# Optimization experiments

Hardware: AMD Instinct MI355X
Metric: run time of the kernel (lower is better)

## Reference

```python
import jax, jax.numpy as jnp
import numpy as np

D = 1024
H = 16
HD = D // H  # 64


def setup_inputs() -> dict:
    key = jax.random.key(0)
    ks = jax.random.split(key, 12)
    B, S = 2, 2048
    inp = {
        "input_query": jax.random.normal(ks[0], (B, S, D), jnp.float32),
        "input_key": jax.random.normal(ks[1], (B, S, D), jnp.float32),
        "input_value": jax.random.normal(ks[2], (B, S, D), jnp.float32),
        "mask": jnp.ones((S, S), dtype=bool),  # ignored, as in original
        # per-head Q/K/V linears, stacked over heads: [H, D, HD]
        "Wq": jax.random.normal(ks[3], (H, D, HD), jnp.float32) / np.sqrt(D),
        "bq": jax.random.normal(ks[4], (H, HD), jnp.float32) * 0.01,
        "Wk": jax.random.normal(ks[5], (H, D, HD), jnp.float32) / np.sqrt(D),
        "bk": jax.random.normal(ks[6], (H, HD), jnp.float32) * 0.01,
        "Wv": jax.random.normal(ks[7], (H, D, HD), jnp.float32) / np.sqrt(D),
        "bv": jax.random.normal(ks[8], (H, HD), jnp.float32) * 0.01,
        "Wo": jax.random.normal(ks[9], (D, D), jnp.float32) / np.sqrt(D),
        "bo": jax.random.normal(ks[10], (D,), jnp.float32) * 0.01,
    }
    return inp


def reference(input_query, input_key, input_value, mask, Wq, bq, Wk, bk, Wv, bv, Wo, bo):
    B, S, _ = input_query.shape
    # batched per-head projections: [B,S,D] x [H,D,HD] -> [B,H,S,HD]
    q = jnp.einsum("bsd,hdk->bhsk", input_query, Wq) + bq[None, :, None, :]
    k = jnp.einsum("bsd,hdk->bhsk", input_key, Wk) + bk[None, :, None, :]
    v = jnp.einsum("bsd,hdk->bhsk", input_value, Wv) + bv[None, :, None, :]
    scale = 1.0 / np.sqrt(HD)
    scores = jnp.einsum("bhqk,bhsk->bhqs", q, k) * scale  # [B,H,S,S]
    causal = jnp.tril(jnp.ones((S, S), dtype=bool))
    scores = jnp.where(causal[None, None], scores, jnp.finfo(scores.dtype).min)
    p = jax.nn.softmax(scores, axis=-1)
    out = jnp.einsum("bhqs,bhsk->bhqk", p, v)  # [B,H,S,HD]
    # concat heads (matches torch.cat over head outputs on last dim)
    out = out.transpose(0, 2, 1, 3).reshape(B, S, D)
    return out @ Wo + bo
```

## Files before the change

kernel.cpp:

```cpp
#include <hip/hip_runtime.h>
#include <hip/hip_bf16.h>

typedef __bf16 bf16;
typedef bf16 bf16x8 __attribute__((ext_vector_type(8)));
typedef bf16 bf16x4 __attribute__((ext_vector_type(4)));
typedef float f32x4 __attribute__((ext_vector_type(4)));

#define B_  2
#define S_  2048
#define D_  1024
#define H_  16
#define HD_ 64
#define M_  4096
#define K_  1024
#define N_  1024

#if __has_builtin(__builtin_amdgcn_exp2f)
#define EXP2F(x) __builtin_amdgcn_exp2f(x)
#else
#define EXP2F(x) exp2f(x)
#endif

__device__ __forceinline__ void gld16(const bf16* g, bf16* l) {
    __builtin_amdgcn_global_load_lds(
        (const __attribute__((address_space(1))) unsigned int*)(g),
        (__attribute__((address_space(3))) unsigned int*)(l), 16, 0, 0);
}


__global__ void pack_x(const float* __restrict__ xq, const float* __restrict__ xk,
                       const float* __restrict__ xv, bf16* __restrict__ out) {
    int t = blockIdx.y;
    const float* src = (t == 0) ? xq : (t == 1) ? xk : xv;
    bf16* dst = out + (size_t)t * M_ * K_;
    int idx = (blockIdx.x * 256 + threadIdx.x) * 4;
    float4 v = *(const float4*)&src[idx];
    bf16x4 o = { (bf16)v.x, (bf16)v.y, (bf16)v.z, (bf16)v.w };
    *(bf16x4*)&dst[idx] = o;
}

__global__ void pack_w(const float* __restrict__ wq, const float* __restrict__ wk,
                       const float* __restrict__ wv, const float* __restrict__ wo,
                       bf16* __restrict__ out) {
    int t = blockIdx.y;
    bf16* dst = out + (size_t)t * N_ * K_;
    int o = blockIdx.x * 256 + threadIdx.x;
    int n = o >> 10, k = o & 1023;
    if (t == 3) {
        dst[o] = (bf16)wo[k * D_ + n];
    } else {
        const float* src = (t == 0) ? wq : (t == 1) ? wk : wv;
        dst[o] = (bf16)src[(n >> 6) * (D_ * HD_) + k * HD_ + (n & 63)];
    }
}

__global__ __launch_bounds__(256) void gemm_qkv(
        const bf16* __restrict__ X, const bf16* __restrict__ Wt,
        const float* __restrict__ bq, const float* __restrict__ bk,
        const float* __restrict__ bv, bf16* __restrict__ QKV) {
    __shared__ __align__(16) bf16 As[2][128 * 32];
    __shared__ __align__(16) bf16 Bs[2][128 * 32];
    int t = blockIdx.z;
    const bf16* A = X + (size_t)t * M_ * K_;
    const bf16* W = Wt + (size_t)t * N_ * K_;
    const float* bias = (t == 0) ? bq : (t == 1) ? bk : bv;
    int m0 = blockIdx.x * 128, n0 = blockIdx.y * 128;
    int tid = threadIdx.x;
    int w = tid >> 6, l = tid & 63, lr = l & 15, lg = l >> 4;
    int wr = (w >> 1) * 64, wc = (w & 1) * 64;
    int srow = (l >> 2), scol = (l & 3) * 8;
    f32x4 acc[4][4] = {};
    #pragma unroll
    for (int c = 0; c < 2; c++) {
        int chunk = w * 2 + c;
        gld16(&A[(size_t)(m0 + chunk * 16 + srow) * K_ + scol], &As[0][chunk * 512]);
        gld16(&W[(size_t)(n0 + chunk * 16 + srow) * K_ + scol], &Bs[0][chunk * 512]);
    }
    __syncthreads();
    for (int k0 = 0; k0 < K_; k0 += 32) {
        int cur = (k0 >> 5) & 1, nxt = cur ^ 1;
        if (k0 + 32 < K_) {
            #pragma unroll
            for (int c = 0; c < 2; c++) {
                int chunk = w * 2 + c;
                gld16(&A[(size_t)(m0 + chunk * 16 + srow) * K_ + k0 + 32 + scol], &As[nxt][chunk * 512]);
                gld16(&W[(size_t)(n0 + chunk * 16 + srow) * K_ + k0 + 32 + scol], &Bs[nxt][chunk * 512]);
            }
        }
        bf16x8 af[4], bfr[4];
        #pragma unroll
        for (int mi = 0; mi < 4; mi++) af[mi] = *(const bf16x8*)&As[cur][(wr + mi * 16 + lr) * 32 + lg * 8];
        #pragma unroll
        for (int ni = 0; ni < 4; ni++) bfr[ni] = *(const bf16x8*)&Bs[cur][(wc + ni * 16 + lr) * 32 + lg * 8];
        #pragma unroll
        for (int mi = 0; mi < 4; mi++)
            #pragma unroll
            for (int ni = 0; ni < 4; ni++)
                acc[mi][ni] = __builtin_amdgcn_mfma_f32_16x16x32_bf16(af[mi], bfr[ni], acc[mi][ni], 0, 0, 0);
        __syncthreads();
    }
    float qscale = (t == 0) ? 0.125f * 1.4426950408889634f : 1.0f;
    #pragma unroll
    for (int mi = 0; mi < 4; mi++)
        #pragma unroll
        for (int ni = 0; ni < 4; ni++)
            #pragma unroll
            for (int i = 0; i < 4; i++) {
                int m = m0 + wr + mi * 16 + lg * 4 + i;
                int n = n0 + wc + ni * 16 + lr;
                float v = (acc[mi][ni][i] + bias[n]) * qscale;
                int b = m >> 11, s = m & 2047, h = n >> 6, hd = n & 63;
                QKV[((((size_t)t * B_ + b) * H_ + h) * S_ + s) * HD_ + hd] = (bf16)v;
            }
}

__global__ __launch_bounds__(256) void gemm_out(
        const bf16* __restrict__ A, const bf16* __restrict__ Wt,
        const float* __restrict__ bo, float* __restrict__ out) {
    __shared__ __align__(16) bf16 As[2][128 * 32];
    __shared__ __align__(16) bf16 Bs[2][128 * 32];
    int m0 = blockIdx.x * 128, n0 = blockIdx.y * 128;
    int tid = threadIdx.x;
    int w = tid >> 6, l = tid & 63, lr = l & 15, lg = l >> 4;
    int wr = (w >> 1) * 64, wc = (w & 1) * 64;
    int srow = (l >> 2), scol = (l & 3) * 8;
    f32x4 acc[4][4] = {};
    #pragma unroll
    for (int c = 0; c < 2; c++) {
        int chunk = w * 2 + c;
        gld16(&A[(size_t)(m0 + chunk * 16 + srow) * K_ + scol], &As[0][chunk * 512]);
        gld16(&Wt[(size_t)(n0 + chunk * 16 + srow) * K_ + scol], &Bs[0][chunk * 512]);
    }
    __syncthreads();
    for (int k0 = 0; k0 < K_; k0 += 32) {
        int cur = (k0 >> 5) & 1, nxt = cur ^ 1;
        if (k0 + 32 < K_) {
            #pragma unroll
            for (int c = 0; c < 2; c++) {
                int chunk = w * 2 + c;
                gld16(&A[(size_t)(m0 + chunk * 16 + srow) * K_ + k0 + 32 + scol], &As[nxt][chunk * 512]);
                gld16(&Wt[(size_t)(n0 + chunk * 16 + srow) * K_ + k0 + 32 + scol], &Bs[nxt][chunk * 512]);
            }
        }
        bf16x8 af[4], bfr[4];
        #pragma unroll
        for (int mi = 0; mi < 4; mi++) af[mi] = *(const bf16x8*)&As[cur][(wr + mi * 16 + lr) * 32 + lg * 8];
        #pragma unroll
        for (int ni = 0; ni < 4; ni++) bfr[ni] = *(const bf16x8*)&Bs[cur][(wc + ni * 16 + lr) * 32 + lg * 8];
        #pragma unroll
        for (int mi = 0; mi < 4; mi++)
            #pragma unroll
            for (int ni = 0; ni < 4; ni++)
                acc[mi][ni] = __builtin_amdgcn_mfma_f32_16x16x32_bf16(af[mi], bfr[ni], acc[mi][ni], 0, 0, 0);
        __syncthreads();
    }
    #pragma unroll
    for (int mi = 0; mi < 4; mi++)
        #pragma unroll
        for (int ni = 0; ni < 4; ni++)
            #pragma unroll
            for (int i = 0; i < 4; i++) {
                int m = m0 + wr + mi * 16 + lg * 4 + i;
                int n = n0 + wc + ni * 16 + lr;
                out[(size_t)m * N_ + n] = acc[mi][ni][i] + bo[n];
            }
}

__global__ __launch_bounds__(256) void transpose_v(const bf16* __restrict__ V,
                                                   bf16* __restrict__ VT) {
    __shared__ __align__(16) bf16 Ls[64][64];
    int s0 = blockIdx.x * 64, bh = blockIdx.y;
    const bf16* src = V + (size_t)bh * S_ * HD_;
    bf16* dst = VT + (size_t)bh * HD_ * S_;
    int tid = threadIdx.x;
    #pragma unroll
    for (int c = tid; c < 512; c += 256) {
        int row = c >> 3, cg = (c & 7) * 8;
        int cgp = cg ^ (((row >> 3) & 3) << 4);
        *(bf16x8*)&Ls[row][cgp] = *(const bf16x8*)&src[(size_t)(s0 + row) * 64 + cg];
    }
    __syncthreads();
    #pragma unroll
    for (int c = tid; c < 512; c += 256) {
        int hd = c >> 3, sg = (c & 7) * 8;
        bf16x8 v;
        #pragma unroll
        for (int e = 0; e < 8; e++) {
            int row = sg + e;
            v[e] = Ls[row][hd ^ (((row >> 3) & 3) << 4)];
        }
        *(bf16x8*)&dst[(size_t)hd * S_ + s0 + sg] = v;
    }
}

__global__ __launch_bounds__(512) void attn(const bf16* __restrict__ QKV,
                                            const bf16* __restrict__ VT,
                                            bf16* __restrict__ AO) {
    __shared__ __align__(16) bf16 Ks[2][64][72];
    __shared__ __align__(16) bf16 Vts[2][64][72];
    __shared__ __align__(16) bf16 Ps[8][16][72];
    int bh = blockIdx.y;
    int qt = (bh & 16) ? blockIdx.x : (15 - blockIdx.x);
    int q0 = qt * 128;
    const bf16* Qp = QKV + (size_t)bh * S_ * HD_;
    const bf16* Kp = QKV + (size_t)(32 + bh) * S_ * HD_;
    const bf16* VTp = VT + (size_t)bh * HD_ * S_;
    int tid = threadIdx.x, w = tid >> 6, l = tid & 63, lr = l & 15, lg = l >> 4;
    int srow = tid >> 3, scg = (tid & 7) * 8;

    bf16x8 aq[2];
    #pragma unroll
    for (int ks = 0; ks < 2; ks++)
        aq[ks] = *(const bf16x8*)&Qp[(size_t)(q0 + w * 16 + lr) * 64 + ks * 32 + lg * 8];

    f32x4 o[4] = {};
    float lsum[4] = {};
    int jmax = 2 * qt + 1;

    *(bf16x8*)&Ks[0][srow][scg]  = *(const bf16x8*)&Kp[(size_t)srow * 64 + scg];
    *(bf16x8*)&Vts[0][srow][scg] = *(const bf16x8*)&VTp[(size_t)srow * S_ + scg];
    __syncthreads();

    for (int j = 0; j <= jmax; ++j) {
        int cur = j & 1;
        bool pf = (j < jmax);
        bf16x8 kreg, vreg;
        if (pf) {
            kreg = *(const bf16x8*)&Kp[(size_t)((j + 1) * 64 + srow) * 64 + scg];
            vreg = *(const bf16x8*)&VTp[(size_t)srow * S_ + (j + 1) * 64 + scg];
        }

        f32x4 sc[4] = {};
        __builtin_amdgcn_s_setprio(1);
        #pragma unroll
        for (int ks = 0; ks < 2; ks++)
            #pragma unroll
            for (int ni = 0; ni < 4; ni++) {
                bf16x8 bk_ = *(const bf16x8*)&Ks[cur][ni * 16 + lr][ks * 32 + lg * 8];
                sc[ni] = __builtin_amdgcn_mfma_f32_16x16x32_bf16(aq[ks], bk_, sc[ni], 0, 0, 0);
            }
        __builtin_amdgcn_s_setprio(0);

        bool diag = (j >= 2 * qt);
        int qrow = w * 16 + lg * 4;
        int kvb = j * 64 - q0;
        #pragma unroll
        for (int ni = 0; ni < 4; ni++)
            #pragma unroll
            for (int i = 0; i < 4; i++) {
                float s = sc[ni][i];
                if (diag && (kvb + ni * 16 + lr > qrow + i)) s = -30000.0f;
                float p = EXP2F(s);
                lsum[i] += p;
                Ps[w][lg * 4 + i][ni * 16 + lr] = (bf16)p;
            }

        __builtin_amdgcn_s_setprio(1);
        #pragma unroll
        for (int ks = 0; ks < 2; ks++) {
            bf16x8 ap = *(const bf16x8*)&Ps[w][lr][ks * 32 + lg * 8];
            #pragma unroll
            for (int nf = 0; nf < 4; nf++) {
                bf16x8 bv_ = *(const bf16x8*)&Vts[cur][nf * 16 + lr][ks * 32 + lg * 8];
                o[nf] = __builtin_amdgcn_mfma_f32_16x16x32_bf16(ap, bv_, o[nf], 0, 0, 0);
            }
        }
        __builtin_amdgcn_s_setprio(0);

        if (pf) {
            *(bf16x8*)&Ks[cur ^ 1][srow][scg]  = kreg;
            *(bf16x8*)&Vts[cur ^ 1][srow][scg] = vreg;
        }
        __syncthreads();
    }

    #pragma unroll
    for (int i = 0; i < 4; i++) {
        #pragma unroll
        for (int xm = 1; xm < 16; xm <<= 1) lsum[i] += __shfl_xor(lsum[i], xm);
    }

    int b = bh >> 4, h = bh & 15;
    #pragma unroll
    for (int i = 0; i < 4; i++) {
        float inv = 1.0f / lsum[i];
        #pragma unroll
        for (int nf = 0; nf < 4; nf++) {
            int m = b * S_ + q0 + w * 16 + lg * 4 + i;
            int d = h * 64 + nf * 16 + lr;
            AO[(size_t)m * D_ + d] = (bf16)(o[nf][i] * inv);
        }
    }
}

extern "C" void kernel_launch(void* const* d_in, const int* in_sizes, int n_in,
                              void* d_out, int out_size, void* d_ws, size_t ws_size,
                              hipStream_t stream) {
    const float* xq = (const float*)d_in[0];
    const float* xk = (const float*)d_in[1];
    const float* xv = (const float*)d_in[2];
    const float* wq = (const float*)d_in[4];
    const float* bq = (const float*)d_in[5];
    const float* wk = (const float*)d_in[6];
    const float* bk = (const float*)d_in[7];
    const float* wv = (const float*)d_in[8];
    const float* bv = (const float*)d_in[9];
    const float* wo = (const float*)d_in[10];
    const float* bo = (const float*)d_in[11];
    float* out = (float*)d_out;

    bf16* Xb  = (bf16*)d_ws;
    bf16* Wb  = Xb  + (size_t)3 * M_ * K_;
    bf16* WoT = Wb  + (size_t)3 * N_ * K_;
    bf16* QKV = WoT + (size_t)N_ * K_;
    bf16* AO  = QKV + (size_t)3 * M_ * K_;
    bf16* VT  = Xb;

    pack_x <<<dim3(M_ * K_ / 1024, 3), 256, 0, stream>>>(xq, xk, xv, Xb);
    pack_w <<<dim3(N_ * K_ / 256, 4), 256, 0, stream>>>(wq, wk, wv, wo, Wb);
    gemm_qkv<<<dim3(M_ / 128, N_ / 128, 3), 256, 0, stream>>>(Xb, Wb, bq, bk, bv, QKV);
    transpose_v<<<dim3(S_ / 64, B_ * H_), 256, 0, stream>>>(QKV + (size_t)2 * M_ * K_, VT);
    attn    <<<dim3(S_ / 128, B_ * H_), 512, 0, stream>>>(QKV, VT, AO);
    gemm_out<<<dim3(M_ / 128, N_ / 128), 256, 0, stream>>>(AO, WoT, bo, out);
}
```

Baseline: 138.7 us.

## Restructure attention to 4 waves with 32 query rows each and swizzled LDS

The attention kernel now runs 256 threads per block, and each wave handles two 16-row query tiles. K and V fragments are loaded from LDS once and reused across both tiles. The padded LDS arrays become XOR-swizzled unpadded layouts. Waves skip KV tiles that lie fully above the causal diagonal for their rows, and masking is applied only where needed. The aim is less LDS traffic per MFMA and less wasted work on the diagonal, at the cost of more registers per thread (launch bounds ask for 3 blocks per CU).

```diff
diff --git a/kernel.cpp b/kernel.cpp
--- a/kernel.cpp
+++ b/kernel.cpp
@@ -193,12 +193,12 @@
     }
 }
 
-__global__ __launch_bounds__(512) void attn(const bf16* __restrict__ QKV,
-                                            const bf16* __restrict__ VT,
-                                            bf16* __restrict__ AO) {
-    __shared__ __align__(16) bf16 Ks[2][64][72];
-    __shared__ __align__(16) bf16 Vts[2][64][72];
-    __shared__ __align__(16) bf16 Ps[8][16][72];
+__global__ __launch_bounds__(256, 3) void attn(const bf16* __restrict__ QKV,
+                                               const bf16* __restrict__ VT,
+                                               bf16* __restrict__ AO) {
+    __shared__ __align__(16) bf16 Ks[2][64 * 64];
+    __shared__ __align__(16) bf16 Vs[2][64 * 64];
+    __shared__ __align__(16) bf16 Ps[4][32 * 64];
     int bh = blockIdx.y;
     int qt = (bh & 16) ? blockIdx.x : (15 - blockIdx.x);
     int q0 = qt * 128;
@@ -206,91 +206,136 @@
     const bf16* Kp = QKV + (size_t)(32 + bh) * S_ * HD_;
     const bf16* VTp = VT + (size_t)bh * HD_ * S_;
     int tid = threadIdx.x, w = tid >> 6, l = tid & 63, lr = l & 15, lg = l >> 4;
-    int srow = tid >> 3, scg = (tid & 7) * 8;
-
-    bf16x8 aq[2];
-    #pragma unroll
-    for (int ks = 0; ks < 2; ks++)
-        aq[ks] = *(const bf16x8*)&Qp[(size_t)(q0 + w * 16 + lr) * 64 + ks * 32 + lg * 8];
-
-    f32x4 o[4] = {};
-    float lsum[4] = {};
+    int rswz = (lr & 7) << 4;
+
+    int srow0 = tid >> 3, scol0 = tid & 7;
+    int srow1 = (tid + 256) >> 3, scol1 = tid & 7;
+    int sdst0 = srow0 * 128 + ((scol0 * 16) ^ ((srow0 & 7) << 4));
+    int sdst1 = srow1 * 128 + ((scol1 * 16) ^ ((srow1 & 7) << 4));
+    const bf16* kg0 = Kp + srow0 * 64 + scol0 * 8;
+    const bf16* kg1 = Kp + srow1 * 64 + scol1 * 8;
+    const bf16* vg0 = VTp + (size_t)srow0 * S_ + scol0 * 8;
+    const bf16* vg1 = VTp + (size_t)srow1 * S_ + scol1 * 8;
+
+    bf16x8 aq[2][2];
+    #pragma unroll
+    for (int t = 0; t < 2; t++)
+        #pragma unroll
+        for (int ks = 0; ks < 2; ks++)
+            aq[t][ks] = *(const bf16x8*)&Qp[(size_t)(q0 + w * 32 + t * 16 + lr) * 64 + ks * 32 + lg * 8];
+
+    f32x4 o[2][4] = {};
+    float lsum[2][4] = {};
     int jmax = 2 * qt + 1;
 
-    *(bf16x8*)&Ks[0][srow][scg]  = *(const bf16x8*)&Kp[(size_t)srow * 64 + scg];
-    *(bf16x8*)&Vts[0][srow][scg] = *(const bf16x8*)&VTp[(size_t)srow * S_ + scg];
+    *(bf16x8*)((char*)Ks[0] + sdst0) = *(const bf16x8*)kg0;
+    *(bf16x8*)((char*)Ks[0] + sdst1) = *(const bf16x8*)kg1;
+    *(bf16x8*)((char*)Vs[0] + sdst0) = *(const bf16x8*)vg0;
+    *(bf16x8*)((char*)Vs[0] + sdst1) = *(const bf16x8*)vg1;
     __syncthreads();
+
+    char* pw = (char*)Ps[w];
 
     for (int j = 0; j <= jmax; ++j) {
         int cur = j & 1;
         bool pf = (j < jmax);
-        bf16x8 kreg, vreg;
+        bf16x8 kr0, kr1, vr0, vr1;
         if (pf) {
-            kreg = *(const bf16x8*)&Kp[(size_t)((j + 1) * 64 + srow) * 64 + scg];
-            vreg = *(const bf16x8*)&VTp[(size_t)srow * S_ + (j + 1) * 64 + scg];
-        }
-
-        f32x4 sc[4] = {};
-        __builtin_amdgcn_s_setprio(1);
-        #pragma unroll
-        for (int ks = 0; ks < 2; ks++)
-            #pragma unroll
-            for (int ni = 0; ni < 4; ni++) {
-                bf16x8 bk_ = *(const bf16x8*)&Ks[cur][ni * 16 + lr][ks * 32 + lg * 8];
-                sc[ni] = __builtin_amdgcn_mfma_f32_16x16x32_bf16(aq[ks], bk_, sc[ni], 0, 0, 0);
-            }
-        __builtin_amdgcn_s_setprio(0);
-
-        bool diag = (j >= 2 * qt);
-        int qrow = w * 16 + lg * 4;
+            kr0 = *(const bf16x8*)(kg0 + (size_t)(j + 1) * 4096);
+            kr1 = *(const bf16x8*)(kg1 + (size_t)(j + 1) * 4096);
+            vr0 = *(const bf16x8*)(vg0 + (j + 1) * 64);
+            vr1 = *(const bf16x8*)(vg1 + (j + 1) * 64);
+        }
+
         int kvb = j * 64 - q0;
-        #pragma unroll
-        for (int ni = 0; ni < 4; ni++)
-            #pragma unroll
-            for (int i = 0; i < 4; i++) {
-                float s = sc[ni][i];
-                if (diag && (kvb + ni * 16 + lr > qrow + i)) s = -30000.0f;
-                float p = EXP2F(s);
-                lsum[i] += p;
-                Ps[w][lg * 4 + i][ni * 16 + lr] = (bf16)p;
-            }
-
-        __builtin_amdgcn_s_setprio(1);
-        #pragma unroll
-        for (int ks = 0; ks < 2; ks++) {
-            bf16x8 ap = *(const bf16x8*)&Ps[w][lr][ks * 32 + lg * 8];
+        if (kvb <= w * 32 + 31) {
+            char* kb = (char*)Ks[cur];
+            bf16x8 bk[2][4];
+            #pragma unroll
+            for (int ks = 0; ks < 2; ks++)
+                #pragma unroll
+                for (int ni = 0; ni < 4; ni++)
+                    bk[ks][ni] = *(const bf16x8*)(kb + (ni * 16 + lr) * 128 + ((ks * 64 + lg * 16) ^ rswz));
+
+            #pragma unroll
+            for (int t = 0; t < 2; t++) {
+                f32x4 sc[4] = {};
+                __builtin_amdgcn_s_setprio(1);
+                #pragma unroll
+                for (int ks = 0; ks < 2; ks++)
+                    #pragma unroll
+                    for (int ni = 0; ni < 4; ni++)
+                        sc[ni] = __builtin_amdgcn_mfma_f32_16x16x32_bf16(aq[t][ks], bk[ks][ni], sc[ni], 0, 0, 0);
+                __builtin_amdgcn_s_setprio(0);
+
+                bool domask = (kvb + 63 > w * 32 + t * 16);
+                int qrow = w * 32 + t * 16 + lg * 4;
+                #pragma unroll
+                for (int ni = 0; ni < 4; ni++)
+                    #pragma unroll
+                    for (int i = 0; i < 4; i++) {
+                        float s = sc[ni][i];
+                        if (domask && (kvb + ni * 16 + lr > qrow + i)) s = -30000.0f;
+                        float p = EXP2F(s);
+                        lsum[t][i] += p;
+                        int prow = t * 16 + lg * 4 + i;
+                        *(bf16*)(pw + prow * 128 + ((ni * 32 + lr * 2) ^ ((prow & 7) << 4))) = (bf16)p;
+                    }
+            }
+
+            char* vb = (char*)Vs[cur];
+            bf16x8 bv[2][4];
+            #pragma unroll
+            for (int ks = 0; ks < 2; ks++)
+                #pragma unroll
+                for (int nf = 0; nf < 4; nf++)
+                    bv[ks][nf] = *(const bf16x8*)(vb + (nf * 16 + lr) * 128 + ((ks * 64 + lg * 16) ^ rswz));
+
+            __builtin_amdgcn_s_setprio(1);
+            #pragma unroll
+            for (int t = 0; t < 2; t++)
+                #pragma unroll
+                for (int ks = 0; ks < 2; ks++) {
+                    bf16x8 ap = *(const bf16x8*)(pw + (t * 16 + lr) * 128 + ((ks * 64 + lg * 16) ^ rswz));
+                    #pragma unroll
+                    for (int nf = 0; nf < 4; nf++)
+                        o[t][nf] = __builtin_amdgcn_mfma_f32_16x16x32_bf16(ap, bv[ks][nf], o[t][nf], 0, 0, 0);
+                }
+            __builtin_amdgcn_s_setprio(0);
+        }
+
+        if (pf) {
+            char* kn = (char*)Ks[cur ^ 1];
+            char* vn = (char*)Vs[cur ^ 1];
+            *(bf16x8*)(kn + sdst0) = kr0;
+            *(bf16x8*)(kn + sdst1) = kr1;
+            *(bf16x8*)(vn + sdst0) = vr0;
+            *(bf16x8*)(vn + sdst1) = vr1;
+        }
+        __syncthreads();
+    }
+
+    #pragma unroll
+    for (int t = 0; t < 2; t++)
+        #pragma unroll
+        for (int i = 0; i < 4; i++) {
+            #pragma unroll
+            for (int xm = 1; xm < 16; xm <<= 1) lsum[t][i] += __shfl_xor(lsum[t][i], xm);
+        }
+
+    int b = bh >> 4, h = bh & 15;
+    #pragma unroll
+    for (int t = 0; t < 2; t++)
+        #pragma unroll
+        for (int i = 0; i < 4; i++) {
+            float inv = 1.0f / lsum[t][i];
             #pragma unroll
             for (int nf = 0; nf < 4; nf++) {
-                bf16x8 bv_ = *(const bf16x8*)&Vts[cur][nf * 16 + lr][ks * 32 + lg * 8];
-                o[nf] = __builtin_amdgcn_mfma_f32_16x16x32_bf16(ap, bv_, o[nf], 0, 0, 0);
-            }
-        }
-        __builtin_amdgcn_s_setprio(0);
-
-        if (pf) {
-            *(bf16x8*)&Ks[cur ^ 1][srow][scg]  = kreg;
-            *(bf16x8*)&Vts[cur ^ 1][srow][scg] = vreg;
-        }
-        __syncthreads();
-    }
-
-    #pragma unroll
-    for (int i = 0; i < 4; i++) {
-        #pragma unroll
-        for (int xm = 1; xm < 16; xm <<= 1) lsum[i] += __shfl_xor(lsum[i], xm);
-    }
-
-    int b = bh >> 4, h = bh & 15;
-    #pragma unroll
-    for (int i = 0; i < 4; i++) {
-        float inv = 1.0f / lsum[i];
-        #pragma unroll
-        for (int nf = 0; nf < 4; nf++) {
-            int m = b * S_ + q0 + w * 16 + lg * 4 + i;
-            int d = h * 64 + nf * 16 + lr;
-            AO[(size_t)m * D_ + d] = (bf16)(o[nf][i] * inv);
-        }
-    }
+                int m = b * S_ + q0 + w * 32 + t * 16 + lg * 4 + i;
+                int d = h * 64 + nf * 16 + lr;
+                AO[(size_t)m * D_ + d] = (bf16)(o[t][nf][i] * inv);
+            }
+        }
 }
 
 extern "C" void kernel_launch(void* const* d_in, const int* in_sizes, int n_in,
@@ -320,6 +365,6 @@
     pack_w <<<dim3(N_ * K_ / 256, 4), 256, 0, stream>>>(wq, wk, wv, wo, Wb);
     gemm_qkv<<<dim3(M_ / 128, N_ / 128, 3), 256, 0, stream>>>(Xb, Wb, bq, bk, bv, QKV);
     transpose_v<<<dim3(S_ / 64, B_ * H_), 256, 0, stream>>>(QKV + (size_t)2 * M_ * K_, VT);
-    attn    <<<dim3(S_ / 128, B_ * H_), 512, 0, stream>>>(QKV, VT, AO);
+    attn    <<<dim3(S_ / 128, B_ * H_), 256, 0, stream>>>(QKV, VT, AO);
     gemm_out<<<dim3(M_ / 128, N_ / 128), 256, 0, stream>>>(AO, WoT, bo, out);
 }
```

Result: slower. 173.8 us (+25.3%).
